# Performance work log

Hardware: AMD Instinct MI355X
Metric: run time of the kernel (lower is better)

Reference implementation:

```python
import jax, jax.numpy as jnp
import numpy as np

B, T, E, H = 1, 2048, 2048, 32
D = E // H  # head_dim = 64


def alibi_bias(n_heads, t_q, t_k, dtype):
    # slopes: 2^(-8*(h+1)/n_heads) for power-of-two head counts
    slopes = jnp.power(2.0, -8.0 * jnp.arange(1, n_heads + 1, dtype=jnp.float32) / n_heads)
    i = jnp.arange(t_q)[:, None] + (t_k - t_q)  # absolute query positions
    j = jnp.arange(t_k)[None, :]
    rel = (j - i).astype(dtype)                 # [t_q, t_k], <=0 on/below diagonal
    return (slopes[:, None, None] * rel).astype(dtype)  # [H, t_q, t_k]


def setup_inputs() -> dict:
    key = jax.random.key(0)
    kx, kq, kk, kv, ko = jax.random.split(key, 5)
    s = E ** -0.5
    x = jax.random.normal(kx, (B, T, E), dtype=jnp.float32)
    Wq = jax.random.normal(kq, (E, E), dtype=jnp.float32) * s
    Wk = jax.random.normal(kk, (D, E), dtype=jnp.float32) * s
    Wv = jax.random.normal(kv, (D, E), dtype=jnp.float32) * s
    Wo = jax.random.normal(ko, (E, E), dtype=jnp.float32) * s
    # causal mask: True where attention is disallowed (j > i)
    attention_mask = jnp.triu(jnp.ones((T, T), dtype=bool), k=1)[None, None]  # [1,1,T,T]
    return {"x": x, "Wq": Wq, "Wk": Wk, "Wv": Wv, "Wo": Wo, "attention_mask": attention_mask}


def reference(x, Wq, Wk, Wv, Wo, attention_mask):
    b, t, _ = x.shape
    scale = D ** -0.5
    q = (x @ Wq.T).reshape(b, t, H, D).transpose(0, 2, 1, 3)  # [b,H,t,D]
    k = x @ Wk.T                                              # [b,t,D] (single KV head)
    v = x @ Wv.T                                              # [b,t,D]
    attn = jnp.einsum('bhtd,bsd->bhts', q * scale, k)         # [b,H,t,t]
    attn = attn + alibi_bias(H, t, t, attn.dtype)[None]
    attn = jnp.where(attention_mask, jnp.asarray(-10000.0, attn.dtype), attn)
    w = jax.nn.softmax(attn, axis=-1)
    out = jnp.einsum('bhts,bsd->bhtd', w, v)                  # [b,H,t,D]
    out = out.transpose(0, 2, 1, 3).reshape(b, t, E)
    return out @ Wo.T
```

## Files before the change

### kernel.cpp

```cpp
#include <hip/hip_runtime.h>
#include <stdint.h>
#include <math.h>

typedef __bf16 bf16;
typedef __bf16 bf16x4 __attribute__((ext_vector_type(4)));
typedef __bf16 bf16x8 __attribute__((ext_vector_type(8)));
typedef short short4v __attribute__((ext_vector_type(4)));
typedef float floatx4 __attribute__((ext_vector_type(4)));

#define MFMA32(a, b, c) __builtin_amdgcn_mfma_f32_16x16x32_bf16((a), (b), (c), 0, 0, 0)

__device__ __forceinline__ floatx4 mfma16(bf16x4 a, bf16x4 b, floatx4 c) {
  return __builtin_amdgcn_mfma_f32_16x16x16bf16_1k(
      __builtin_bit_cast(short4v, a), __builtin_bit_cast(short4v, b), c, 0, 0, 0);
}

__device__ __forceinline__ void gload16(const void* g, void* l) {
  __builtin_amdgcn_global_load_lds(
      (const __attribute__((address_space(1))) void*)g,
      (__attribute__((address_space(3))) void*)l, 16, 0, 0);
}

__device__ __forceinline__ bf16x8 load8(const float* p) {
  float4 lo = *(const float4*)p;
  float4 hi = *(const float4*)(p + 4);
  bf16x8 r;
  r[0] = (bf16)lo.x; r[1] = (bf16)lo.y; r[2] = (bf16)lo.z; r[3] = (bf16)lo.w;
  r[4] = (bf16)hi.x; r[5] = (bf16)hi.y; r[6] = (bf16)hi.z; r[7] = (bf16)hi.w;
  return r;
}

__global__ __launch_bounds__(256) void conv3(const float* __restrict__ a, bf16* __restrict__ ab,
                                             const float* __restrict__ b, bf16* __restrict__ bb,
                                             const float* __restrict__ c, bf16* __restrict__ cb) {
  const int i = blockIdx.x * 256 + threadIdx.x;
  const float* src = blockIdx.y == 0 ? a : (blockIdx.y == 1 ? b : c);
  bf16* dst = blockIdx.y == 0 ? ab : (blockIdx.y == 1 ? bb : cb);
  ((bf16x8*)dst)[i] = load8(src + (size_t)i * 8);
}

__global__ __launch_bounds__(256) void pack_kv(const float* __restrict__ Kf,
                                               const float* __restrict__ Vf,
                                               bf16* __restrict__ Kb,
                                               bf16* __restrict__ Vtb) {
  int i = blockIdx.x * 256 + threadIdx.x;
  if (i < 2048 * 64) {
    Kb[i] = (bf16)Kf[i];
    const int t = i >> 6, d = i & 63;
    Vtb[(size_t)d * 2048 + t] = (bf16)Vf[i];
  }
}

template <typename TC>
__global__ __launch_bounds__(256) void gemm_bt_a(const bf16* __restrict__ A,
                                                 const bf16* __restrict__ B,
                                                 TC* __restrict__ C,
                                                 int M, int N, int K) {
  __shared__ __align__(16) bf16 As[2][64 * 32];
  __shared__ __align__(16) bf16 Bs[2][128 * 32];
  const int tid = threadIdx.x;
  const int wave = tid >> 6, lane = tid & 63;
  const int quad = lane >> 4, l16 = lane & 15;
  const int m0 = blockIdx.y * 64, n0 = blockIdx.x * 128;
  const int wm = (wave >> 1) * 32, wn = (wave & 1) * 64;

  floatx4 acc[2][4];
#pragma unroll
  for (int i = 0; i < 2; i++)
#pragma unroll
    for (int j = 0; j < 4; j++) acc[i][j] = (floatx4)0.f;

  const int srow = tid >> 2;
  const int scol = ((tid & 3) ^ ((tid >> 3) & 3)) * 8;
  const bf16* Ap = A + (size_t)(m0 + srow) * K + scol;
  const bf16* Bp = B + (size_t)(n0 + srow) * K + scol;

  auto stage = [&](int k0, int buf) {
    gload16(Ap + k0, (char*)As[buf] + tid * 16);
    gload16(Bp + k0, (char*)Bs[buf] + tid * 16);
    gload16(Bp + (size_t)64 * K + k0, (char*)Bs[buf] + 4096 + tid * 16);
  };
  const int sxg = (l16 >> 1) & 3;
  auto compute = [&](int buf) {
    bf16x8 af[2], bfr[4];
#pragma unroll
    for (int mt = 0; mt < 2; mt++)
      af[mt] = *(const bf16x8*)(&As[buf][(wm + mt * 16 + l16) * 32 + ((quad ^ sxg) * 8)]);
#pragma unroll
    for (int nt = 0; nt < 4; nt++)
      bfr[nt] = *(const bf16x8*)(&Bs[buf][(wn + nt * 16 + l16) * 32 + ((quad ^ sxg) * 8)]);
#pragma unroll
    for (int mt = 0; mt < 2; mt++)
#pragma unroll
      for (int nt = 0; nt < 4; nt++)
        acc[mt][nt] = MFMA32(af[mt], bfr[nt], acc[mt][nt]);
  };

  stage(0, 0);
  for (int k0 = 0; k0 < K; k0 += 64) {
    __syncthreads();
    if (k0 + 32 < K) stage(k0 + 32, 1);
    compute(0);
    __syncthreads();
    if (k0 + 64 < K) stage(k0 + 64, 0);
    compute(1);
  }

#pragma unroll
  for (int mt = 0; mt < 2; mt++) {
#pragma unroll
    for (int nt = 0; nt < 4; nt++) {
      const int col = n0 + wn + nt * 16 + l16;
      const int row = m0 + wm + mt * 16 + quad * 4;
#pragma unroll
      for (int r = 0; r < 4; r++)
        C[(size_t)(row + r) * N + col] = (TC)acc[mt][nt][r];
    }
  }
}

__global__ __launch_bounds__(256) void kv_gemm(const bf16* __restrict__ xb,
                                               const float* __restrict__ Wk,
                                               const float* __restrict__ Wv,
                                               float* __restrict__ Kf,
                                               float* __restrict__ Vf) {
  __shared__ __align__(16) bf16 As[128 * 40];
  __shared__ __align__(16) bf16 Bs[128 * 40];
  const int tid = threadIdx.x;
  const int wave = tid >> 6, lane = tid & 63;
  const int quad = lane >> 4, l16 = lane & 15;
  const int m0 = blockIdx.y * 128;
  const int kbeg = blockIdx.x * 256, kend = kbeg + 256;
  const int wm = (wave >> 1) * 64, wn = (wave & 1) * 64;

  floatx4 acc[4][4];
#pragma unroll
  for (int i = 0; i < 4; i++)
#pragma unroll
    for (int j = 0; j < 4; j++) acc[i][j] = (floatx4)0.f;

  const int sr = tid >> 2, sc = (tid & 3) * 8;

  for (int k0 = kbeg; k0 < kend; k0 += 32) {
    __syncthreads();
#pragma unroll
    for (int rr = 0; rr < 2; rr++) {
      const int row = sr + rr * 64;
      *(bf16x8*)(&As[row * 40 + sc]) =
          *(const bf16x8*)(&xb[(size_t)(m0 + row) * 2048 + k0 + sc]);
      const float* bsrc = (row < 64) ? &Wk[(size_t)row * 2048 + k0 + sc]
                                     : &Wv[(size_t)(row - 64) * 2048 + k0 + sc];
      *(bf16x8*)(&Bs[row * 40 + sc]) = load8(bsrc);
    }
    __syncthreads();

    bf16x8 af[4], bfr[4];
#pragma unroll
    for (int mt = 0; mt < 4; mt++)
      af[mt] = *(const bf16x8*)(&As[(wm + mt * 16 + l16) * 40 + quad * 8]);
#pragma unroll
    for (int nt = 0; nt < 4; nt++)
      bfr[nt] = *(const bf16x8*)(&Bs[(wn + nt * 16 + l16) * 40 + quad * 8]);
#pragma unroll
    for (int mt = 0; mt < 4; mt++)
#pragma unroll
      for (int nt = 0; nt < 4; nt++)
        acc[mt][nt] = MFMA32(af[mt], bfr[nt], acc[mt][nt]);
  }

#pragma unroll
  for (int mt = 0; mt < 4; mt++) {
#pragma unroll
    for (int nt = 0; nt < 4; nt++) {
      const int col = wn + nt * 16 + l16;
      const int row = m0 + wm + mt * 16 + quad * 4;
      float* dst = (col < 64) ? &Kf[(size_t)row * 64 + col]
                              : &Vf[(size_t)row * 64 + (col - 64)];
#pragma unroll
      for (int r = 0; r < 4; r++) atomicAdd(dst + (size_t)r * 64, acc[mt][nt][r]);
    }
  }
}

#define WTHR 30.f

__global__ __launch_bounds__(1024) void mktable(uint32_t* __restrict__ tbl) {
  __shared__ int bins[17], base[17];
  const int i = threadIdx.x;
  const int p = i & 511, hf = i >> 9;
  const int h = p & 31, t = p >> 5;
  const float slope2 = exp2f(-0.25f * (float)(h + 1)) * 1.44269504f;
  const int lo_key = t * 128 - (int)(WTHR / slope2);
  const int lo_t = (lo_key <= 0) ? 0 : (lo_key >> 6);
  const int m = 2 * t + 2 - lo_t;
  const int load = hf ? (m >> 1) : ((m + 1) >> 1);
  if (i < 17) bins[i] = 0;
  __syncthreads();
  atomicAdd(&bins[load], 1);
  __syncthreads();
  if (i == 0) {
    int s = 0;
    for (int v = 16; v >= 0; --v) { base[v] = s; s += bins[v]; }
  }
  __syncthreads();
  if (i < 17) bins[i] = 0;
  __syncthreads();
  const int off = atomicAdd(&bins[load], 1);
  const int rank = base[load] + off;
  tbl[rank] = ((uint32_t)hf << 9) | (uint32_t)p;
}

__global__ __launch_bounds__(512) void attn_kernel(const bf16* __restrict__ Q,
                                                   const bf16* __restrict__ Kb,
                                                   const bf16* __restrict__ Vtb,
                                                   float* __restrict__ OpA,
                                                   float* __restrict__ OpB,
                                                   float* __restrict__ lpart,
                                                   const uint32_t* __restrict__ tbl) {
  __shared__ __align__(16) bf16 Ks[2][64 * 64];
  __shared__ __align__(16) bf16 Vt[2][64 * 64];

  const int u = blockIdx.x & 255, sfold = blockIdx.x >> 8;
  const int r = (sfold == 0) ? u : (sfold == 1) ? (511 - u)
                : (sfold == 2) ? (512 + u) : (1023 - u);
  const uint32_t e = tbl[r];
  const int p = e & 511, hf = (int)(e >> 9);
  const int h = p & 31, t = p >> 5;

  const float slope2 = exp2f(-0.25f * (float)(h + 1)) * 1.44269504f;
  const int lo_key = t * 128 - (int)(WTHR / slope2);
  const int lo_t = (lo_key <= 0) ? 0 : (lo_key >> 6);
  const int m = 2 * t + 2 - lo_t;
  const int c0 = (m + 1) >> 1;
  const int kbeg = hf ? (lo_t + c0) : lo_t;
  const int cnt = hf ? (m >> 1) : c0;

  const int tid = threadIdx.x;
  const int wave = tid >> 6;
  const int lane = tid & 63;
  const int quad = lane >> 4, l16 = lane & 15;
  const float scale2 = 0.125f * 1.44269504f;
  const bf16x4 ones = {(bf16)1.f, (bf16)1.f, (bf16)1.f, (bf16)1.f};

  float cq[4];
#pragma unroll
  for (int rr = 0; rr < 4; rr++) cq[rr] = slope2 * (float)(quad * 4 + rr);
  const float s16 = slope2 * 16.f;

  const int qi = t * 128 + wave * 16 + l16;
  const int qw0 = t * 128 + wave * 16;
  bf16x8 qf[2];
#pragma unroll
  for (int kk = 0; kk < 2; kk++)
    qf[kk] = *(const bf16x8*)(&Q[(size_t)qi * 2048 + h * 64 + kk * 32 + quad * 8]);

  floatx4 oacc[4];
#pragma unroll
  for (int dt = 0; dt < 4; dt++) oacc[dt] = (floatx4)0.f;
  floatx4 lacc = (floatx4)0.f;

  const int r0 = tid >> 3, sl = tid & 7;
  const int wsw = ((sl ^ (r0 & 7)) << 3);
  const int sx = l16 & 7;

  const int kn = kbeg * 64;
  bf16x8 kreg = *(const bf16x8*)(&Kb[(size_t)(kn + r0) * 64 + sl * 8]);
  bf16x8 vreg = *(const bf16x8*)(&Vtb[(size_t)r0 * 2048 + kn + sl * 8]);

  for (int i = 0; i < cnt; i++) {
    const int kt = kbeg + i;
    const int buf = i & 1;
    *(bf16x8*)(&Ks[buf][r0 * 64 + wsw]) = kreg;
    *(bf16x8*)(&Vt[buf][r0 * 64 + wsw]) = vreg;
    __syncthreads();
    if (i + 1 < cnt) {
      const int kn2 = (kt + 1) * 64;
      kreg = *(const bf16x8*)(&Kb[(size_t)(kn2 + r0) * 64 + sl * 8]);
      vreg = *(const bf16x8*)(&Vtb[(size_t)r0 * 2048 + kn2 + sl * 8]);
    }
    const int k0 = kt * 64;
    if (k0 > qw0 + 15) continue;
    if ((float)(qw0 - k0 - 63) * slope2 > WTHR) continue;

    const bf16* ks = Ks[buf];
    const bf16* vs = Vt[buf];

    floatx4 s[4];
#pragma unroll
    for (int mt = 0; mt < 4; mt++) s[mt] = (floatx4)0.f;
#pragma unroll
    for (int kk = 0; kk < 2; kk++) {
#pragma unroll
      for (int mt = 0; mt < 4; mt++) {
        bf16x8 kf = *(const bf16x8*)(
            &ks[(mt * 16 + l16) * 64 + (((kk * 4 + quad) ^ sx) << 3)]);
        s[mt] = MFMA32(kf, qf[kk], s[mt]);
      }
    }

    const float base0 = slope2 * (float)(k0 - qi);
    bf16x4 pb[4];
    if (k0 + 63 <= qw0) {
      float b = base0;
#pragma unroll
      for (int mt = 0; mt < 4; mt++) {
        bf16x4 tb;
#pragma unroll
        for (int rr = 0; rr < 4; rr++)
          tb[rr] = (bf16)exp2f(__builtin_fmaf(s[mt][rr], scale2, b + cq[rr]));
        pb[mt] = tb;
        b += s16;
      }
    } else {
      const int qloc = qi - k0;
      float b = base0;
#pragma unroll
      for (int mt = 0; mt < 4; mt++) {
        bf16x4 tb;
#pragma unroll
        for (int rr = 0; rr < 4; rr++) {
          const int moff = mt * 16 + quad * 4 + rr;
          const float pv = exp2f(__builtin_fmaf(s[mt][rr], scale2, b + cq[rr]));
          tb[rr] = (moff <= qloc) ? (bf16)pv : (bf16)0.f;
        }
        pb[mt] = tb;
        b += s16;
      }
    }

#pragma unroll
    for (int mt = 0; mt < 4; mt++) {
      lacc = mfma16(ones, pb[mt], lacc);
#pragma unroll
      for (int dt = 0; dt < 4; dt++) {
        const int slot = 2 * mt + (quad >> 1);
        const bf16x4 va = *(const bf16x4*)(
            &vs[(dt * 16 + l16) * 64 + ((slot ^ sx) << 3) + (quad & 1) * 4]);
        oacc[dt] = mfma16(va, pb[mt], oacc[dt]);
      }
    }
  }

  float* op = (hf ? OpB : OpA) + (size_t)qi * 2048 + h * 64;
#pragma unroll
  for (int dt = 0; dt < 4; dt++)
#pragma unroll
    for (int rr = 0; rr < 4; rr++)
      op[dt * 16 + quad * 4 + rr] = oacc[dt][rr];
  if (quad == 0) lpart[(size_t)hf * 65536 + (size_t)qi * 32 + h] = lacc[0];
}

__global__ __launch_bounds__(256) void norm_o(const float* __restrict__ P0,
                                              const float* __restrict__ P1,
                                              const float* __restrict__ L,
                                              bf16* __restrict__ AO) {
  const int idx = blockIdx.x * 256 + threadIdx.x;
  const int qi = idx >> 8;
  const int cs = (idx & 255) << 3;
  const int h = cs >> 6;
  const float l = L[(size_t)qi * 32 + h] + L[65536 + (size_t)qi * 32 + h];
  const float linv = 1.f / l;
  const float4 a0 = *(const float4*)(P0 + (size_t)qi * 2048 + cs);
  const float4 a1 = *(const float4*)(P0 + (size_t)qi * 2048 + cs + 4);
  const float4 b0 = *(const float4*)(P1 + (size_t)qi * 2048 + cs);
  const float4 b1 = *(const float4*)(P1 + (size_t)qi * 2048 + cs + 4);
  bf16x8 o;
  o[0] = (bf16)((a0.x + b0.x) * linv); o[1] = (bf16)((a0.y + b0.y) * linv);
  o[2] = (bf16)((a0.z + b0.z) * linv); o[3] = (bf16)((a0.w + b0.w) * linv);
  o[4] = (bf16)((a1.x + b1.x) * linv); o[5] = (bf16)((a1.y + b1.y) * linv);
  o[6] = (bf16)((a1.z + b1.z) * linv); o[7] = (bf16)((a1.w + b1.w) * linv);
  *(bf16x8*)(AO + (size_t)qi * 2048 + cs) = o;
}

extern "C" void kernel_launch(void* const* d_in, const int* in_sizes, int n_in,
                              void* d_out, int out_size, void* d_ws,
                              size_t ws_size, hipStream_t stream) {
  (void)in_sizes; (void)n_in; (void)out_size; (void)ws_size;
  const float* x = (const float*)d_in[0];
  const float* Wq = (const float*)d_in[1];
  const float* Wk = (const float*)d_in[2];
  const float* Wv = (const float*)d_in[3];
  const float* Wo = (const float*)d_in[4];
  float* out = (float*)d_out;

  const size_t NE = (size_t)2048 * 2048;
  bf16* xb = (bf16*)d_ws;
  bf16* Wqb = xb + NE;
  bf16* Wob = Wqb + NE;
  bf16* Qb = Wob + NE;
  float* Kf = (float*)(Qb + NE);
  float* Vf = Kf + 2048 * 64;
  bf16* Kb = (bf16*)(Vf + 2048 * 64);
  bf16* Vtb = Kb + 2048 * 64;
  float* OpA = (float*)d_ws;
  float* OpB = out;
  float* lpart = Kf;
  uint32_t* tbl = (uint32_t*)Vf;
  bf16* AO = Qb;

  hipMemsetAsync(Kf, 0, 2 * 2048 * 64 * sizeof(float), stream);
  conv3<<<dim3(2048, 3), 256, 0, stream>>>(x, xb, Wq, Wqb, Wo, Wob);
  gemm_bt_a<bf16><<<dim3(16, 32), 256, 0, stream>>>(xb, Wqb, Qb, 2048, 2048, 2048);
  kv_gemm<<<dim3(8, 16), 256, 0, stream>>>(xb, Wk, Wv, Kf, Vf);
  pack_kv<<<512, 256, 0, stream>>>(Kf, Vf, Kb, Vtb);
  mktable<<<1, 1024, 0, stream>>>(tbl);
  attn_kernel<<<1024, 512, 0, stream>>>(Qb, Kb, Vtb, OpA, OpB, lpart, tbl);
  norm_o<<<2048, 256, 0, stream>>>(OpA, OpB, lpart, AO);
  gemm_bt_a<float><<<dim3(16, 32), 256, 0, stream>>>(AO, Wob, out, 2048, 2048, 2048);
}
```

Before: 236.5 us.

## Use persistent atomic work queue with 64-row query tiles in attention

The attention kernel now works on 64-query-row items with 256-thread blocks instead of 128-row items with 512 threads. 1280 persistent blocks pull items from a load-sorted table through a global atomic counter, replacing the fixed block-to-item mapping. The aim is better load balance across the uneven causal/ALiBi-windowed work and less idle time at the tail. The cost is an atomic fetch and two barriers per item, and each K/V tile is now loaded once per 64 query rows rather than once per 128.

```diff
diff --git a/kernel.cpp b/kernel.cpp
--- a/kernel.cpp
+++ b/kernel.cpp
@@ -184,56 +184,56 @@
 
 #define WTHR 30.f
 
+__device__ __forceinline__ int item_cnt(int h, int t, int hf, int hq) {
+  const float slope2 = exp2f(-0.25f * (float)(h + 1)) * 1.44269504f;
+  const int q0 = t * 128 + hq * 64;
+  const int lo_key = q0 - (int)(WTHR / slope2);
+  const int lo_t = (lo_key <= 0) ? 0 : (lo_key >> 6);
+  const int end = 2 * t + 1 + hq;
+  const int m = end - lo_t;
+  const int c0 = (m + 1) >> 1;
+  return hf ? (m - c0) : c0;
+}
+
 __global__ __launch_bounds__(1024) void mktable(uint32_t* __restrict__ tbl) {
   __shared__ int bins[17], base[17];
-  const int i = threadIdx.x;
-  const int p = i & 511, hf = i >> 9;
-  const int h = p & 31, t = p >> 5;
-  const float slope2 = exp2f(-0.25f * (float)(h + 1)) * 1.44269504f;
-  const int lo_key = t * 128 - (int)(WTHR / slope2);
-  const int lo_t = (lo_key <= 0) ? 0 : (lo_key >> 6);
-  const int m = 2 * t + 2 - lo_t;
-  const int load = hf ? (m >> 1) : ((m + 1) >> 1);
-  if (i < 17) bins[i] = 0;
+  const int i0 = threadIdx.x;
+  if (i0 < 17) bins[i0] = 0;
   __syncthreads();
-  atomicAdd(&bins[load], 1);
+  int loads[2];
+#pragma unroll
+  for (int k = 0; k < 2; k++) {
+    const int idx = i0 + k * 1024;
+    loads[k] = item_cnt(idx & 31, (idx >> 5) & 15, (idx >> 9) & 1, (idx >> 10) & 1);
+    atomicAdd(&bins[loads[k]], 1);
+  }
   __syncthreads();
-  if (i == 0) {
+  if (i0 == 0) {
     int s = 0;
     for (int v = 16; v >= 0; --v) { base[v] = s; s += bins[v]; }
+    tbl[0] = 0;
   }
   __syncthreads();
-  if (i < 17) bins[i] = 0;
+  if (i0 < 17) bins[i0] = 0;
   __syncthreads();
-  const int off = atomicAdd(&bins[load], 1);
-  const int rank = base[load] + off;
-  tbl[rank] = ((uint32_t)hf << 9) | (uint32_t)p;
-}
-
-__global__ __launch_bounds__(512) void attn_kernel(const bf16* __restrict__ Q,
+#pragma unroll
+  for (int k = 0; k < 2; k++) {
+    const int idx = i0 + k * 1024;
+    const int off = atomicAdd(&bins[loads[k]], 1);
+    tbl[1 + base[loads[k]] + off] = (uint32_t)idx;
+  }
+}
+
+__global__ __launch_bounds__(256) void attn_kernel(const bf16* __restrict__ Q,
                                                    const bf16* __restrict__ Kb,
                                                    const bf16* __restrict__ Vtb,
                                                    float* __restrict__ OpA,
                                                    float* __restrict__ OpB,
                                                    float* __restrict__ lpart,
-                                                   const uint32_t* __restrict__ tbl) {
+                                                   uint32_t* __restrict__ tbl) {
   __shared__ __align__(16) bf16 Ks[2][64 * 64];
   __shared__ __align__(16) bf16 Vt[2][64 * 64];
-
-  const int u = blockIdx.x & 255, sfold = blockIdx.x >> 8;
-  const int r = (sfold == 0) ? u : (sfold == 1) ? (511 - u)
-                : (sfold == 2) ? (512 + u) : (1023 - u);
-  const uint32_t e = tbl[r];
-  const int p = e & 511, hf = (int)(e >> 9);
-  const int h = p & 31, t = p >> 5;
-
-  const float slope2 = exp2f(-0.25f * (float)(h + 1)) * 1.44269504f;
-  const int lo_key = t * 128 - (int)(WTHR / slope2);
-  const int lo_t = (lo_key <= 0) ? 0 : (lo_key >> 6);
-  const int m = 2 * t + 2 - lo_t;
-  const int c0 = (m + 1) >> 1;
-  const int kbeg = hf ? (lo_t + c0) : lo_t;
-  const int cnt = hf ? (m >> 1) : c0;
+  __shared__ uint32_t curit;
 
   const int tid = threadIdx.x;
   const int wave = tid >> 6;
@@ -242,112 +242,146 @@
   const float scale2 = 0.125f * 1.44269504f;
   const bf16x4 ones = {(bf16)1.f, (bf16)1.f, (bf16)1.f, (bf16)1.f};
 
-  float cq[4];
-#pragma unroll
-  for (int rr = 0; rr < 4; rr++) cq[rr] = slope2 * (float)(quad * 4 + rr);
-  const float s16 = slope2 * 16.f;
-
-  const int qi = t * 128 + wave * 16 + l16;
-  const int qw0 = t * 128 + wave * 16;
-  bf16x8 qf[2];
-#pragma unroll
-  for (int kk = 0; kk < 2; kk++)
-    qf[kk] = *(const bf16x8*)(&Q[(size_t)qi * 2048 + h * 64 + kk * 32 + quad * 8]);
-
-  floatx4 oacc[4];
-#pragma unroll
-  for (int dt = 0; dt < 4; dt++) oacc[dt] = (floatx4)0.f;
-  floatx4 lacc = (floatx4)0.f;
-
-  const int r0 = tid >> 3, sl = tid & 7;
-  const int wsw = ((sl ^ (r0 & 7)) << 3);
+  const int r0 = tid >> 2, sl2 = (tid & 3) << 1;
+  const int wsw0 = ((sl2 ^ (r0 & 7)) << 3);
+  const int wsw1 = (((sl2 + 1) ^ (r0 & 7)) << 3);
   const int sx = l16 & 7;
 
-  const int kn = kbeg * 64;
-  bf16x8 kreg = *(const bf16x8*)(&Kb[(size_t)(kn + r0) * 64 + sl * 8]);
-  bf16x8 vreg = *(const bf16x8*)(&Vtb[(size_t)r0 * 2048 + kn + sl * 8]);
-
-  for (int i = 0; i < cnt; i++) {
-    const int kt = kbeg + i;
-    const int buf = i & 1;
-    *(bf16x8*)(&Ks[buf][r0 * 64 + wsw]) = kreg;
-    *(bf16x8*)(&Vt[buf][r0 * 64 + wsw]) = vreg;
-    __syncthreads();
-    if (i + 1 < cnt) {
-      const int kn2 = (kt + 1) * 64;
-      kreg = *(const bf16x8*)(&Kb[(size_t)(kn2 + r0) * 64 + sl * 8]);
-      vreg = *(const bf16x8*)(&Vtb[(size_t)r0 * 2048 + kn2 + sl * 8]);
-    }
-    const int k0 = kt * 64;
-    if (k0 > qw0 + 15) continue;
-    if ((float)(qw0 - k0 - 63) * slope2 > WTHR) continue;
-
-    const bf16* ks = Ks[buf];
-    const bf16* vs = Vt[buf];
-
-    floatx4 s[4];
-#pragma unroll
-    for (int mt = 0; mt < 4; mt++) s[mt] = (floatx4)0.f;
-#pragma unroll
-    for (int kk = 0; kk < 2; kk++) {
-#pragma unroll
-      for (int mt = 0; mt < 4; mt++) {
-        bf16x8 kf = *(const bf16x8*)(
-            &ks[(mt * 16 + l16) * 64 + (((kk * 4 + quad) ^ sx) << 3)]);
-        s[mt] = MFMA32(kf, qf[kk], s[mt]);
+  uint32_t* const counter = tbl;
+  const uint32_t* const items = tbl + 1;
+
+  for (;;) {
+    if (tid == 0) curit = atomicAdd(counter, 1u);
+    __syncthreads();
+    const uint32_t r = curit;
+    __syncthreads();
+    if (r >= 2048u) return;
+    const uint32_t e = items[r];
+    const int h = e & 31, t = (e >> 5) & 15;
+    const int hf = (e >> 9) & 1, hq = (e >> 10) & 1;
+
+    const float slope2 = exp2f(-0.25f * (float)(h + 1)) * 1.44269504f;
+    const int q0 = t * 128 + hq * 64;
+    const int lo_key = q0 - (int)(WTHR / slope2);
+    const int lo_t = (lo_key <= 0) ? 0 : (lo_key >> 6);
+    const int end = 2 * t + 1 + hq;
+    const int m = end - lo_t;
+    const int c0 = (m + 1) >> 1;
+    const int kbeg = hf ? (lo_t + c0) : lo_t;
+    const int cnt = hf ? (m - c0) : c0;
+
+    const int qi = q0 + wave * 16 + l16;
+    const int qw0 = q0 + wave * 16;
+
+    floatx4 oacc[4];
+#pragma unroll
+    for (int dt = 0; dt < 4; dt++) oacc[dt] = (floatx4)0.f;
+    floatx4 lacc = (floatx4)0.f;
+
+    if (cnt > 0) {
+      float cq[4];
+#pragma unroll
+      for (int rr = 0; rr < 4; rr++) cq[rr] = slope2 * (float)(quad * 4 + rr);
+      const float s16 = slope2 * 16.f;
+
+      bf16x8 qf[2];
+#pragma unroll
+      for (int kk = 0; kk < 2; kk++)
+        qf[kk] = *(const bf16x8*)(&Q[(size_t)qi * 2048 + h * 64 + kk * 32 + quad * 8]);
+
+      int kn = kbeg * 64;
+      bf16x8 ka = *(const bf16x8*)(&Kb[(size_t)(kn + r0) * 64 + sl2 * 8]);
+      bf16x8 kb2 = *(const bf16x8*)(&Kb[(size_t)(kn + r0) * 64 + sl2 * 8 + 8]);
+      bf16x8 va = *(const bf16x8*)(&Vtb[(size_t)r0 * 2048 + kn + sl2 * 8]);
+      bf16x8 vb = *(const bf16x8*)(&Vtb[(size_t)r0 * 2048 + kn + sl2 * 8 + 8]);
+
+      for (int i = 0; i < cnt; i++) {
+        const int kt = kbeg + i;
+        const int buf = i & 1;
+        *(bf16x8*)(&Ks[buf][r0 * 64 + wsw0]) = ka;
+        *(bf16x8*)(&Ks[buf][r0 * 64 + wsw1]) = kb2;
+        *(bf16x8*)(&Vt[buf][r0 * 64 + wsw0]) = va;
+        *(bf16x8*)(&Vt[buf][r0 * 64 + wsw1]) = vb;
+        __syncthreads();
+        if (i + 1 < cnt) {
+          const int kn2 = (kt + 1) * 64;
+          ka = *(const bf16x8*)(&Kb[(size_t)(kn2 + r0) * 64 + sl2 * 8]);
+          kb2 = *(const bf16x8*)(&Kb[(size_t)(kn2 + r0) * 64 + sl2 * 8 + 8]);
+          va = *(const bf16x8*)(&Vtb[(size_t)r0 * 2048 + kn2 + sl2 * 8]);
+          vb = *(const bf16x8*)(&Vtb[(size_t)r0 * 2048 + kn2 + sl2 * 8 + 8]);
+        }
+        const int k0 = kt * 64;
+        if (k0 > qw0 + 15) continue;
+        if ((float)(qw0 - k0 - 63) * slope2 > WTHR) continue;
+
+        const bf16* ks = Ks[buf];
+        const bf16* vs = Vt[buf];
+
+        floatx4 s[4];
+#pragma unroll
+        for (int mt = 0; mt < 4; mt++) s[mt] = (floatx4)0.f;
+#pragma unroll
+        for (int kk = 0; kk < 2; kk++) {
+#pragma unroll
+          for (int mt = 0; mt < 4; mt++) {
+            bf16x8 kf = *(const bf16x8*)(
+                &ks[(mt * 16 + l16) * 64 + (((kk * 4 + quad) ^ sx) << 3)]);
+            s[mt] = MFMA32(kf, qf[kk], s[mt]);
+          }
+        }
+
+        const float base0 = slope2 * (float)(k0 - qi);
+        bf16x4 pb[4];
+        if (k0 + 63 <= qw0) {
+          float b = base0;
+#pragma unroll
+          for (int mt = 0; mt < 4; mt++) {
+            bf16x4 tb;
+#pragma unroll
+            for (int rr = 0; rr < 4; rr++)
+              tb[rr] = (bf16)exp2f(__builtin_fmaf(s[mt][rr], scale2, b + cq[rr]));
+            pb[mt] = tb;
+            b += s16;
+          }
+        } else {
+          const int qloc = qi - k0;
+          float b = base0;
+#pragma unroll
+          for (int mt = 0; mt < 4; mt++) {
+            bf16x4 tb;
+#pragma unroll
+            for (int rr = 0; rr < 4; rr++) {
+              const int moff = mt * 16 + quad * 4 + rr;
+              const float pv = exp2f(__builtin_fmaf(s[mt][rr], scale2, b + cq[rr]));
+              tb[rr] = (moff <= qloc) ? (bf16)pv : (bf16)0.f;
+            }
+            pb[mt] = tb;
+            b += s16;
+          }
+        }
+
+#pragma unroll
+        for (int mt = 0; mt < 4; mt++) {
+          lacc = mfma16(ones, pb[mt], lacc);
+#pragma unroll
+          for (int dt = 0; dt < 4; dt++) {
+            const int slot = 2 * mt + (quad >> 1);
+            const bf16x4 vv = *(const bf16x4*)(
+                &vs[(dt * 16 + l16) * 64 + ((slot ^ sx) << 3) + (quad & 1) * 4]);
+            oacc[dt] = mfma16(vv, pb[mt], oacc[dt]);
+          }
+        }
       }
     }
 
-    const float base0 = slope2 * (float)(k0 - qi);
-    bf16x4 pb[4];
-    if (k0 + 63 <= qw0) {
-      float b = base0;
-#pragma unroll
-      for (int mt = 0; mt < 4; mt++) {
-        bf16x4 tb;
-#pragma unroll
-        for (int rr = 0; rr < 4; rr++)
-          tb[rr] = (bf16)exp2f(__builtin_fmaf(s[mt][rr], scale2, b + cq[rr]));
-        pb[mt] = tb;
-        b += s16;
-      }
-    } else {
-      const int qloc = qi - k0;
-      float b = base0;
-#pragma unroll
-      for (int mt = 0; mt < 4; mt++) {
-        bf16x4 tb;
-#pragma unroll
-        for (int rr = 0; rr < 4; rr++) {
-          const int moff = mt * 16 + quad * 4 + rr;
-          const float pv = exp2f(__builtin_fmaf(s[mt][rr], scale2, b + cq[rr]));
-          tb[rr] = (moff <= qloc) ? (bf16)pv : (bf16)0.f;
-        }
-        pb[mt] = tb;
-        b += s16;
-      }
-    }
-
-#pragma unroll
-    for (int mt = 0; mt < 4; mt++) {
-      lacc = mfma16(ones, pb[mt], lacc);
-#pragma unroll
-      for (int dt = 0; dt < 4; dt++) {
-        const int slot = 2 * mt + (quad >> 1);
-        const bf16x4 va = *(const bf16x4*)(
-            &vs[(dt * 16 + l16) * 64 + ((slot ^ sx) << 3) + (quad & 1) * 4]);
-        oacc[dt] = mfma16(va, pb[mt], oacc[dt]);
-      }
-    }
-  }
-
-  float* op = (hf ? OpB : OpA) + (size_t)qi * 2048 + h * 64;
-#pragma unroll
-  for (int dt = 0; dt < 4; dt++)
-#pragma unroll
-    for (int rr = 0; rr < 4; rr++)
-      op[dt * 16 + quad * 4 + rr] = oacc[dt][rr];
-  if (quad == 0) lpart[(size_t)hf * 65536 + (size_t)qi * 32 + h] = lacc[0];
+    float* op = (hf ? OpB : OpA) + (size_t)qi * 2048 + h * 64;
+#pragma unroll
+    for (int dt = 0; dt < 4; dt++)
+#pragma unroll
+      for (int rr = 0; rr < 4; rr++)
+        op[dt * 16 + quad * 4 + rr] = oacc[dt][rr];
+    if (quad == 0) lpart[(size_t)hf * 65536 + (size_t)qi * 32 + h] = lacc[0];
+  }
 }
 
 __global__ __launch_bounds__(256) void norm_o(const float* __restrict__ P0,
@@ -404,7 +438,7 @@
   kv_gemm<<<dim3(8, 16), 256, 0, stream>>>(xb, Wk, Wv, Kf, Vf);
   pack_kv<<<512, 256, 0, stream>>>(Kf, Vf, Kb, Vtb);
   mktable<<<1, 1024, 0, stream>>>(tbl);
-  attn_kernel<<<1024, 512, 0, stream>>>(Qb, Kb, Vtb, OpA, OpB, lpart, tbl);
+  attn_kernel<<<1280, 256, 0, stream>>>(Qb, Kb, Vtb, OpA, OpB, lpart, tbl);
   norm_o<<<2048, 256, 0, stream>>>(OpA, OpB, lpart, AO);
   gemm_bt_a<float><<<dim3(16, 32), 256, 0, stream>>>(AO, Wob, out, 2048, 2048, 2048);
 }
```

Result: slower. 257.8 us (+9.0%).

## Split-K the Q and output projection GEMMs with atomic fp32 accumulation

Applied to the files above, without the earlier changes.

Replaces the two large projection GEMMs with a split-K variant that divides K into two halves across a third grid dimension and accumulates into fp32 output with atomicAdd. The Q projection now writes fp32 into a scratch buffer that is zeroed first and then converted to bf16 by a new kernel. The aim is to double the number of workgroups to better occupy the GPU, at the cost of extra memsets, atomic traffic, and a conversion pass.

```diff
diff --git a/kernel.cpp b/kernel.cpp
--- a/kernel.cpp
+++ b/kernel.cpp
@@ -37,6 +37,12 @@
   const float* src = blockIdx.y == 0 ? a : (blockIdx.y == 1 ? b : c);
   bf16* dst = blockIdx.y == 0 ? ab : (blockIdx.y == 1 ? bb : cb);
   ((bf16x8*)dst)[i] = load8(src + (size_t)i * 8);
+}
+
+__global__ __launch_bounds__(256) void cvt1(const float* __restrict__ s,
+                                            bf16* __restrict__ d) {
+  const int i = blockIdx.x * 256 + threadIdx.x;
+  ((bf16x8*)d)[i] = load8(s + (size_t)i * 8);
 }
 
 __global__ __launch_bounds__(256) void pack_kv(const float* __restrict__ Kf,
@@ -51,17 +57,18 @@
   }
 }
 
-template <typename TC>
-__global__ __launch_bounds__(256) void gemm_bt_a(const bf16* __restrict__ A,
-                                                 const bf16* __restrict__ B,
-                                                 TC* __restrict__ C,
-                                                 int M, int N, int K) {
+template <int KS>
+__global__ __launch_bounds__(256) void gemm_sk(const bf16* __restrict__ A,
+                                               const bf16* __restrict__ B,
+                                               float* __restrict__ C,
+                                               int M, int N, int K) {
   __shared__ __align__(16) bf16 As[2][64 * 32];
   __shared__ __align__(16) bf16 Bs[2][128 * 32];
   const int tid = threadIdx.x;
   const int wave = tid >> 6, lane = tid & 63;
   const int quad = lane >> 4, l16 = lane & 15;
   const int m0 = blockIdx.y * 64, n0 = blockIdx.x * 128;
+  const int kbase = blockIdx.z * KS;
   const int wm = (wave >> 1) * 32, wn = (wave & 1) * 64;
 
   floatx4 acc[2][4];
@@ -72,8 +79,8 @@
 
   const int srow = tid >> 2;
   const int scol = ((tid & 3) ^ ((tid >> 3) & 3)) * 8;
-  const bf16* Ap = A + (size_t)(m0 + srow) * K + scol;
-  const bf16* Bp = B + (size_t)(n0 + srow) * K + scol;
+  const bf16* Ap = A + (size_t)(m0 + srow) * K + kbase + scol;
+  const bf16* Bp = B + (size_t)(n0 + srow) * K + kbase + scol;
 
   auto stage = [&](int k0, int buf) {
     gload16(Ap + k0, (char*)As[buf] + tid * 16);
@@ -97,12 +104,12 @@
   };
 
   stage(0, 0);
-  for (int k0 = 0; k0 < K; k0 += 64) {
+  for (int k0 = 0; k0 < KS; k0 += 64) {
     __syncthreads();
-    if (k0 + 32 < K) stage(k0 + 32, 1);
+    if (k0 + 32 < KS) stage(k0 + 32, 1);
     compute(0);
     __syncthreads();
-    if (k0 + 64 < K) stage(k0 + 64, 0);
+    if (k0 + 64 < KS) stage(k0 + 64, 0);
     compute(1);
   }
 
@@ -114,7 +121,7 @@
       const int row = m0 + wm + mt * 16 + quad * 4;
 #pragma unroll
       for (int r = 0; r < 4; r++)
-        C[(size_t)(row + r) * N + col] = (TC)acc[mt][nt][r];
+        atomicAdd(&C[(size_t)(row + r) * N + col], acc[mt][nt][r]);
     }
   }
 }
@@ -396,15 +403,19 @@
   float* OpB = out;
   float* lpart = Kf;
   uint32_t* tbl = (uint32_t*)Vf;
+  float* Qf32 = out;
   bf16* AO = Qb;
 
-  hipMemsetAsync(Kf, 0, 2 * 2048 * 64 * sizeof(float), stream);
+  (void)hipMemsetAsync(Kf, 0, 2 * 2048 * 64 * sizeof(float), stream);
+  (void)hipMemsetAsync(Qf32, 0, NE * sizeof(float), stream);
   conv3<<<dim3(2048, 3), 256, 0, stream>>>(x, xb, Wq, Wqb, Wo, Wob);
-  gemm_bt_a<bf16><<<dim3(16, 32), 256, 0, stream>>>(xb, Wqb, Qb, 2048, 2048, 2048);
+  gemm_sk<1024><<<dim3(16, 32, 2), 256, 0, stream>>>(xb, Wqb, Qf32, 2048, 2048, 2048);
+  cvt1<<<2048, 256, 0, stream>>>(Qf32, Qb);
   kv_gemm<<<dim3(8, 16), 256, 0, stream>>>(xb, Wk, Wv, Kf, Vf);
   pack_kv<<<512, 256, 0, stream>>>(Kf, Vf, Kb, Vtb);
   mktable<<<1, 1024, 0, stream>>>(tbl);
   attn_kernel<<<1024, 512, 0, stream>>>(Qb, Kb, Vtb, OpA, OpB, lpart, tbl);
   norm_o<<<2048, 256, 0, stream>>>(OpA, OpB, lpart, AO);
-  gemm_bt_a<float><<<dim3(16, 32), 256, 0, stream>>>(AO, Wob, out, 2048, 2048, 2048);
-}
+  (void)hipMemsetAsync(out, 0, NE * sizeof(float), stream);
+  gemm_sk<1024><<<dim3(16, 32, 2), 256, 0, stream>>>(AO, Wob, out, 2048, 2048, 2048);
+}
```

New measurement: 290.9 us. +23.0%, slower.
